# Performance work log

Measured on AMD Instinct MI355X. Metric: run time of the kernel, lower is better.

Reference implementation:

```python
import math
import jax, jax.numpy as jnp
import numpy as np

D_MODEL = 1024
N_HEADS = 16
D_FF = 4096
B = 4
T = 1024  # tgt len
S = 1024  # src len
EPS = 1e-6


def _linear_params(key, d_in, d_out):
    kw, kb = jax.random.split(key)
    w = jax.random.normal(kw, (d_out, d_in), dtype=jnp.float32) * 0.02
    b = jax.random.normal(kb, (d_out,), dtype=jnp.float32) * 0.02
    return w, b


def setup_inputs() -> dict:
    key = jax.random.key(0)
    ks = jax.random.split(key, 16)
    x = jax.random.normal(ks[0], (B, T, D_MODEL), dtype=jnp.float32)
    memory = jax.random.normal(ks[1], (B, S, D_MODEL), dtype=jnp.float32)
    # causal [B, T, T] mask (dim==3 branch) and padding [B, S] mask (dim==2 branch)
    tgt_mask = jnp.broadcast_to(jnp.tril(jnp.ones((T, T), dtype=jnp.int32)), (B, T, T))
    src_mask = jnp.ones((B, S), dtype=jnp.int32)
    inp = {"x": x, "memory": memory, "tgt_mask": tgt_mask, "src_mask": src_mask}
    names = ["sa_wq", "sa_wk", "sa_wv", "sa_wo", "ca_wq", "ca_wk", "ca_wv", "ca_wo"]
    for i, n in enumerate(names):
        w, b = _linear_params(ks[2 + i], D_MODEL, D_MODEL)
        inp[n] = w
        inp[n.replace("w", "b")] = b
    inp["ff_w1"], inp["ff_b1"] = _linear_params(ks[10], D_MODEL, D_FF)
    inp["ff_w2"], inp["ff_b2"] = _linear_params(ks[11], D_FF, D_MODEL)
    for i, n in enumerate(["ln1", "ln2", "ln3"]):
        inp[n + "_w"] = jnp.ones((D_MODEL,), dtype=jnp.float32)
        inp[n + "_b"] = jnp.zeros((D_MODEL,), dtype=jnp.float32)
    return inp


def layernorm(x, w, b):
    # torch-faithful: unbiased std (N-1), eps added to std (not variance)
    mean = jnp.mean(x, axis=-1, keepdims=True)
    d = x - mean
    std = jnp.sqrt(jnp.sum(d * d, axis=-1, keepdims=True) / (x.shape[-1] - 1))
    return w * d / (std + EPS) + b


def mha(q_in, kv_in, mask, wq, bq, wk, bk, wv, bv, wo, bo):
    Bb, Tq, D = q_in.shape
    Tk = kv_in.shape[1]
    dk = D // N_HEADS
    if mask.ndim == 2:
        mask4 = mask[:, None, None, :]
    else:
        mask4 = mask[:, None, :, :]
    q = (q_in @ wq.T + bq).reshape(Bb, Tq, N_HEADS, dk).transpose(0, 2, 1, 3)
    k = (kv_in @ wk.T + bk).reshape(Bb, Tk, N_HEADS, dk).transpose(0, 2, 1, 3)
    v = (kv_in @ wv.T + bv).reshape(Bb, Tk, N_HEADS, dk).transpose(0, 2, 1, 3)
    scores = jnp.einsum("bhqd,bhkd->bhqk", q, k) / math.sqrt(dk)
    scores = jnp.where(mask4 == 0, jnp.float32(-1e9), scores)
    attn = jax.nn.softmax(scores, axis=-1)
    out = jnp.einsum("bhqk,bhkd->bhqd", attn, v)
    out = out.transpose(0, 2, 1, 3).reshape(Bb, Tq, D)
    return out @ wo.T + bo


def reference(x, memory, tgt_mask, src_mask,
              sa_wq, sa_bq, sa_wk, sa_bk, sa_wv, sa_bv, sa_wo, sa_bo,
              ca_wq, ca_bq, ca_wk, ca_bk, ca_wv, ca_bv, ca_wo, ca_bo,
              ff_w1, ff_b1, ff_w2, ff_b2,
              ln1_w, ln1_b, ln2_w, ln2_b, ln3_w, ln3_b):
    # pre-norm decoder block (norm_first=True), dropout=0 (eval)
    h = layernorm(x, ln1_w, ln1_b)
    x = x + mha(h, h, tgt_mask, sa_wq, sa_bq, sa_wk, sa_bk, sa_wv, sa_bv, sa_wo, sa_bo)
    h = layernorm(x, ln2_w, ln2_b)
    x = x + mha(h, memory, src_mask, ca_wq, ca_bq, ca_wk, ca_bk, ca_wv, ca_bv, ca_wo, ca_bo)
    h = layernorm(x, ln3_w, ln3_b)
    x = x + (jax.nn.relu(h @ ff_w1.T + ff_b1) @ ff_w2.T + ff_b2)
    return x
```

## Files before the change

### kernel.cpp

```cpp
#include <hip/hip_runtime.h>
#include <hip/hip_bf16.h>

typedef unsigned short u16;
typedef __attribute__((ext_vector_type(4))) float f32x4;
typedef __attribute__((ext_vector_type(8))) short s16x8;
typedef __attribute__((ext_vector_type(4))) short s16x4;
typedef __attribute__((ext_vector_type(8))) __bf16 bf16x8;

#define NTOK 4096
#define DMODEL 1024
#define DFF 4096
#define NH 16
#define TSEQ 1024

#define SBAR() do { asm volatile("" ::: "memory"); __builtin_amdgcn_s_barrier(); asm volatile("" ::: "memory"); } while (0)


__device__ __forceinline__ u16 f2b_hw(float f) {
  union { __bf16 h; u16 u; } cv;
  cv.h = (__bf16)f;
  return cv.u;
}

__device__ __forceinline__ float b2f(u16 u) {
  return __uint_as_float(((unsigned)u) << 16);
}

__device__ __forceinline__ f32x4 mfma16(s16x8 a, s16x8 b, f32x4 c) {
  return __builtin_amdgcn_mfma_f32_16x16x32_bf16((bf16x8)a, (bf16x8)b, c, 0, 0, 0);
}

__device__ __forceinline__ void gload16(const u16* g, u16* l) {
  __builtin_amdgcn_global_load_lds(
      (const __attribute__((address_space(1))) unsigned int*)g,
      (__attribute__((address_space(3))) unsigned int*)l, 16, 0, 0);
}

__device__ __forceinline__ s16x8 ld8s(const u16* t, int row, int eoff) {
  int rx = row & 7;
  const u16* p1 = t + row * 64 + ((((eoff >> 3) ^ rx) << 3) | (eoff & 7));
  const u16* p2 = t + row * 64 + (((((eoff + 16) >> 3) ^ rx) << 3) | (eoff & 7));
  s16x4 lo = *(const s16x4*)p1;
  s16x4 hi = *(const s16x4*)p2;
  s16x8 r;
  r[0] = lo[0]; r[1] = lo[1]; r[2] = lo[2]; r[3] = lo[3];
  r[4] = hi[0]; r[5] = hi[1]; r[6] = hi[2]; r[7] = hi[3];
  return r;
}

__device__ __forceinline__ s16x8 ld16s(const u16* t, int row, int ch) {
  return *(const s16x8*)(t + row * 64 + ((ch ^ (row & 7)) << 3));
}


struct F2B {
  const float* s[11];
  u16* d[11];
};

__global__ __launch_bounds__(256) void f2b_all(F2B a) {
  int bid = blockIdx.x;
  int seg, boff;
  if (bid < 8192) { seg = bid >> 10; boff = bid & 1023; }
  else { int j = bid - 8192; seg = 8 + (j >> 12); boff = j & 4095; }
  size_t i = ((size_t)boff * 256 + threadIdx.x) * 4;
  float4 v = *(const float4*)(a.s[seg] + i);
  ushort4 o = make_ushort4(f2b_hw(v.x), f2b_hw(v.y), f2b_hw(v.z), f2b_hw(v.w));
  *(ushort4*)(a.d[seg] + i) = o;
}


__global__ __launch_bounds__(256) void ln_kernel(const float* __restrict__ x,
                                                 const float* __restrict__ w,
                                                 const float* __restrict__ b,
                                                 u16* __restrict__ out) {
  int row = blockIdx.x;
  int t = threadIdx.x;
  const float* xr = x + (size_t)row * DMODEL;
  float4 v = *(const float4*)(xr + t * 4);
  float s = v.x + v.y + v.z + v.w;
#pragma unroll
  for (int off = 1; off < 64; off <<= 1) s += __shfl_xor(s, off);
  __shared__ float red[8];
  int wid = t >> 6, lane = t & 63;
  if (lane == 0) red[wid] = s;
  __syncthreads();
  float mean = (red[0] + red[1] + red[2] + red[3]) * (1.0f / 1024.0f);
  float dx = v.x - mean, dy = v.y - mean, dz = v.z - mean, dw = v.w - mean;
  float ss = dx * dx + dy * dy + dz * dz + dw * dw;
#pragma unroll
  for (int off = 1; off < 64; off <<= 1) ss += __shfl_xor(ss, off);
  if (lane == 0) red[4 + wid] = ss;
  __syncthreads();
  float sst = red[4] + red[5] + red[6] + red[7];
  float inv = 1.0f / (sqrtf(sst / 1023.0f) + 1e-6f);
  float4 wv = *(const float4*)(w + t * 4);
  float4 bv = *(const float4*)(b + t * 4);
  ushort4 o = make_ushort4(f2b_hw(wv.x * dx * inv + bv.x), f2b_hw(wv.y * dy * inv + bv.y),
                           f2b_hw(wv.z * dz * inv + bv.z), f2b_hw(wv.w * dw * inv + bv.w));
  *(ushort4*)(out + (size_t)row * DMODEL + t * 4) = o;
}


template <bool RELU>
__global__ __launch_bounds__(512, 2) void gemm256(const u16* __restrict__ A,
                                                  const u16* __restrict__ W,
                                                  const float* __restrict__ bias,
                                                  u16* __restrict__ out,
                                                  int M, int N, int K, int ld,
                                                  int gx) {
  __shared__ u16 As[2][2][8192];
  __shared__ u16 Bs[2][2][8192];
  const int nwg = gridDim.x, qch = nwg >> 3, bid = blockIdx.x;
  const int wg = (bid & 7) * qch + (bid >> 3);
  const int bx = wg % gx, by = wg / gx;
  const int m0 = by * 256, n0 = bx * 256;
  const int tid = threadIdx.x;
  const int wid = tid >> 6, lane = tid & 63;
  const int wr = wid >> 2, wc = wid & 3;
  const int lhi = lane >> 4, llo = lane & 15;
  f32x4 acc[8][4] = {};
  const int srow = tid >> 2;
  const int ssw = ((tid & 3) ^ ((srow >> 1) & 3)) << 3;

  auto unitA = [&](int kt, int kh) {
    const u16* p = A + (size_t)(m0 + srow) * ld + kt * 64 + kh * 32 + ssw;
    gload16(p, &As[kt & 1][kh][tid * 8]);
    gload16(p + (size_t)128 * ld, &As[kt & 1][kh][4096 + tid * 8]);
  };
  auto unitB = [&](int kt, int kh) {
    const u16* p = W + (size_t)(n0 + srow) * ld + kt * 64 + kh * 32 + ssw;
    gload16(p, &Bs[kt & 1][kh][tid * 8]);
    gload16(p + (size_t)128 * ld, &Bs[kt & 1][kh][4096 + tid * 8]);
  };

  s16x8 bf[4];
  auto phase = [&](int d, int ch, int kh, bool loadB, auto stfn, int vm) {
    s16x8 af[4];
#pragma unroll
    for (int fm = 0; fm < 4; fm++) {
      int row = wr * 128 + ch * 64 + fm * 16 + llo;
      af[fm] = *(const s16x8*)(&As[d][kh][row * 32 + ((lhi ^ ((row >> 1) & 3)) << 3)]);
    }
    if (loadB) {
#pragma unroll
      for (int fn = 0; fn < 4; fn++) {
        int row = wc * 64 + fn * 16 + llo;
        bf[fn] = *(const s16x8*)(&Bs[d][kh][row * 32 + ((lhi ^ ((row >> 1) & 3)) << 3)]);
      }
    }
    stfn();
    SBAR();
    __builtin_amdgcn_s_setprio(1);
#pragma unroll
    for (int fm = 0; fm < 4; fm++)
#pragma unroll
      for (int fn = 0; fn < 4; fn++)
        acc[ch * 4 + fm][fn] = mfma16(af[fm], bf[fn], acc[ch * 4 + fm][fn]);
    __builtin_amdgcn_s_setprio(0);
    if (vm == 8) asm volatile("s_waitcnt vmcnt(8)" ::: "memory");
    else if (vm == 4) asm volatile("s_waitcnt vmcnt(4)" ::: "memory");
    else if (vm == 0) asm volatile("s_waitcnt vmcnt(0)" ::: "memory");
    SBAR();
  };

  unitA(0, 0); unitB(0, 0); unitA(0, 1); unitB(0, 1); unitA(1, 0); unitB(1, 0);
  asm volatile("s_waitcnt vmcnt(8)" ::: "memory");
  SBAR();

  const int NPAIR = K >> 7;
#pragma unroll 1
  for (int i = 0; i < NPAIR; ++i) {
    const int tb = 2 * i + 1, tc = 2 * i + 2, td = 2 * i + 3;
    const bool nx = (i + 1 < NPAIR);
    phase(0, 0, 0, true,  [&] { unitA(tb, 1); }, -1);
    phase(0, 1, 0, false, [&] { unitB(tb, 1); }, 8);
    phase(0, 1, 1, true,  [&] { if (nx) unitA(tc, 0); }, -1);
    phase(0, 0, 1, false, [&] { if (nx) unitB(tc, 0); }, nx ? 8 : 4);
    phase(1, 0, 0, true,  [&] { if (nx) unitA(tc, 1); }, -1);
    phase(1, 1, 0, false, [&] { if (nx) unitB(tc, 1); }, nx ? 8 : 0);
    phase(1, 1, 1, true,  [&] { if (nx) unitA(td, 0); }, -1);
    phase(1, 0, 1, false, [&] { if (nx) unitB(td, 0); }, nx ? 8 : -1);
  }

#pragma unroll
  for (int ch = 0; ch < 2; ch++)
#pragma unroll
    for (int fm = 0; fm < 4; fm++)
#pragma unroll
      for (int fn = 0; fn < 4; fn++) {
        int r0 = m0 + wr * 128 + ch * 64 + fm * 16 + lhi * 4;
        int c = n0 + wc * 64 + fn * 16 + llo;
        float bv = bias[c];
#pragma unroll
        for (int i2 = 0; i2 < 4; i2++) {
          float v = acc[ch * 4 + fm][fn][i2] + bv;
          if (RELU) v = fmaxf(v, 0.0f);
          out[(size_t)(r0 + i2) * N + c] = f2b_hw(v);
        }
      }
  (void)M;
}


template <int MODE, bool RELU, bool SPLITK = false, int QBUF = -1, int VBUF = -1>
__global__ __launch_bounds__(512) void gemm_bt(const u16* __restrict__ A,
                                               const u16* __restrict__ A2,
                                               const u16* __restrict__ W,
                                               const float* __restrict__ b0,
                                               const float* __restrict__ b1,
                                               const float* __restrict__ b2,
                                               const float* resid, void* outp,
                                               int M, int N, int K, int ld,
                                               int gx) {
  __shared__ u16 As[2][128 * 64];
  __shared__ u16 Bs[2][128 * 64];
  const int nwg = gridDim.x;
  const int qch = nwg >> 3;
  const int bid = blockIdx.x;
  int wg = (bid & 7) * qch + (bid >> 3);
  int half = 0;
  if (SPLITK) { half = wg & 1; wg >>= 1; }
  const int bx = wg % gx, by = wg / gx;
  const int m0 = by * 128, n0 = bx * 128;
  if (SPLITK) { A += (size_t)half * K; W += (size_t)half * K; }
  if (MODE == 2 && A2 != nullptr && n0 >= 1024) A = A2;
  const int tid = threadIdx.x;
  const int wid = tid >> 6, lane = tid & 63;
  const int wr = wid >> 2, wc = wid & 3;
  const int lhi = lane >> 4, llo = lane & 15;
  f32x4 acc[4][2] = {};
  const int sr = tid >> 3, sc = tid & 7;
  const int srcoff = (sc ^ (sr & 7)) << 3;

  auto stage = [&](int kk, int buf) {
    const u16* Ap = A + (size_t)(m0 + sr) * ld + kk + srcoff;
    gload16(Ap, &As[buf][tid * 8]);
    gload16(Ap + (size_t)64 * ld, &As[buf][4096 + tid * 8]);
    const u16* Wp = W + (size_t)(n0 + sr) * ld + kk + srcoff;
    gload16(Wp, &Bs[buf][tid * 8]);
    gload16(Wp + (size_t)64 * ld, &Bs[buf][4096 + tid * 8]);
  };

  stage(0, 0);
  __syncthreads();

  for (int k0 = 0; k0 < K; k0 += 64) {
    int cur = (k0 >> 6) & 1;
    if (k0 + 64 < K) stage(k0 + 64, cur ^ 1);
#pragma unroll
    for (int ks8 = 0; ks8 < 8; ks8 += 4) {
      s16x8 af[4], bfr[2];
#pragma unroll
      for (int f = 0; f < 4; f++) af[f] = ld16s(&As[cur][0], wr * 64 + f * 16 + llo, ks8 + lhi);
#pragma unroll
      for (int g = 0; g < 2; g++) bfr[g] = ld16s(&Bs[cur][0], wc * 32 + g * 16 + llo, ks8 + lhi);
#pragma unroll
      for (int f = 0; f < 4; f++)
#pragma unroll
        for (int g = 0; g < 2; g++) acc[f][g] = mfma16(af[f], bfr[g], acc[f][g]);
    }
    __syncthreads();
  }

#pragma unroll
  for (int fm = 0; fm < 4; fm++) {
#pragma unroll
    for (int fn = 0; fn < 2; fn++) {
      int c = n0 + wc * 32 + fn * 16 + llo;
      const int r0 = m0 + wr * 64 + fm * 16 + lhi * 4;
      if (MODE == 2) {
        int buf = c >> 10, cc = c & 1023;
        int hh = cc >> 6, d = cc & 63;
        int bb = r0 >> 10, t0 = r0 & 1023;
        const float* bias = (buf == 0) ? b0 : ((buf == 1) ? b1 : b2);
        float bv = bias[cc];
        float v4[4];
#pragma unroll
        for (int i = 0; i < 4; i++) {
          float v = acc[fm][fn][i] + bv;
          if (buf == QBUF) v *= 0.125f;
          v4[i] = v;
        }
        if (buf == VBUF) {
          ushort4 st = make_ushort4(f2b_hw(v4[0]), f2b_hw(v4[1]), f2b_hw(v4[2]), f2b_hw(v4[3]));
          *(ushort4*)(&((u16*)outp)[(size_t)buf * 4194304 +
                                    (((size_t)(bb * NH + hh)) * 64 + d) * TSEQ + t0]) = st;
        } else {
#pragma unroll
          for (int i = 0; i < 4; i++)
            ((u16*)outp)[(size_t)buf * 4194304 +
                         (((size_t)(bb * NH + hh)) * TSEQ + t0 + i) * 64 + d] = f2b_hw(v4[i]);
        }
      } else if (MODE == 4) {
#pragma unroll
        for (int i = 0; i < 4; i++)
          ((u16*)outp)[(size_t)half * M * N + (size_t)(r0 + i) * N + c] =
              f2b_hw(acc[fm][fn][i]);
      } else {
        float bv = b0 ? b0[c] : 0.0f;
#pragma unroll
        for (int i = 0; i < 4; i++) {
          int r = r0 + i;
          float v = acc[fm][fn][i] + bv;
          if (resid) v += resid[(size_t)r * N + c];
          if (RELU) v = fmaxf(v, 0.0f);
          if (MODE == 0) {
            ((float*)outp)[(size_t)r * N + c] = v;
          } else {
            ((u16*)outp)[(size_t)r * N + c] = f2b_hw(v);
          }
        }
      }
    }
  }
}


__global__ __launch_bounds__(256) void ff2_reduce(const u16* __restrict__ p,
                                                  const float* __restrict__ bias,
                                                  float* __restrict__ out) {
  int row = blockIdx.x, t = threadIdx.x;
  size_t i = (size_t)row * 1024 + t * 4;
  const u16* p1 = p + (size_t)4194304;
  s16x4 a = *(const s16x4*)(p + i);
  s16x4 b = *(const s16x4*)(p1 + i);
  float4 r = *(const float4*)(out + i);
  float4 bv = *(const float4*)(bias + t * 4);
  float4 o = make_float4(b2f((u16)a[0]) + b2f((u16)b[0]) + r.x + bv.x,
                         b2f((u16)a[1]) + b2f((u16)b[1]) + r.y + bv.y,
                         b2f((u16)a[2]) + b2f((u16)b[2]) + r.z + bv.z,
                         b2f((u16)a[3]) + b2f((u16)b[3]) + r.w + bv.w);
  *(float4*)(out + i) = o;
}


template <bool CAUSAL>
__global__ __launch_bounds__(256) void attn_kernel(const u16* __restrict__ Qg,
                                                   const u16* __restrict__ Kg,
                                                   const u16* __restrict__ Vt,
                                                   u16* __restrict__ Og) {
  const int bid = blockIdx.x;
  const int wg = (bid & 7) * 64 + (bid >> 3);
  const int bh = wg >> 3;
  const int qblk = (wg & 7) ^ (CAUSAL ? 7 * ((bid >> 8) & 1) : 0);
  const int b = bh >> 4, h = bh & 15;
  const int q0 = qblk * 128;
  const int tid = threadIdx.x, wid = tid >> 6, lane = tid & 63;
  const int lhi = lane >> 4, llo = lane & 15;
  __shared__ u16 Ks[2][4096];
  __shared__ u16 Vs[2][4096];

  const int qr = q0 + wid * 16 + llo;
  const u16* qp0 = Qg + ((size_t)bh * TSEQ + qr) * 64;
  s16x8 qf[2][2];
  qf[0][0] = *(const s16x8*)(qp0 + 8 * lhi);
  qf[0][1] = *(const s16x8*)(qp0 + 8 * (4 + lhi));
  qf[1][0] = *(const s16x8*)(qp0 + 4096 + 8 * lhi);
  qf[1][1] = *(const s16x8*)(qp0 + 4096 + 8 * (4 + lhi));

  f32x4 oacc[2][4] = {};
  float mrun[2] = {-1.0e30f, -1.0e30f}, lrun[2] = {0.0f, 0.0f};
  const size_t kvb = (size_t)bh * (TSEQ * 64);
  const int nt = CAUSAL ? ((q0 + 128) >> 6) : (TSEQ >> 6);

  const int srow = tid >> 3;
  const int ssw = ((tid & 7) ^ (srow & 7)) << 3;

  auto stageK = [&](int s0, int buf) {
    const u16* kb = Kg + kvb + (size_t)s0 * 64;
    gload16(kb + (size_t)srow * 64 + ssw, &Ks[buf][tid * 8]);
    gload16(kb + (size_t)(32 + srow) * 64 + ssw, &Ks[buf][2048 + tid * 8]);
  };
  auto stageV = [&](int s0, int buf) {
    const u16* vb2 = Vt + kvb + s0;
    gload16(vb2 + (size_t)srow * TSEQ + ssw, &Vs[buf][tid * 8]);
    gload16(vb2 + (size_t)(32 + srow) * TSEQ + ssw, &Vs[buf][2048 + tid * 8]);
  };

  stageK(0, 0);
  stageV(0, 0);
  __syncthreads();

  for (int t = 0; t < nt; ++t) {
    int cur = t & 1;
    if (t + 1 < nt) {
      stageK((t + 1) * 64, cur ^ 1);
      stageV((t + 1) * 64, cur ^ 1);
    }
    int s0 = t * 64;
    const bool act0 = !CAUSAL || (s0 < q0 + 64);

    s16x8 kf[4][2];
#pragma unroll
    for (int g = 0; g < 4; g++) {
      kf[g][0] = ld16s(&Ks[cur][0], g * 16 + llo, lhi);
      kf[g][1] = ld16s(&Ks[cur][0], g * 16 + llo, 4 + lhi);
    }

    s16x8 pf[2][2];
#pragma unroll
    for (int s = 0; s < 2; s++) {
      if (s == 0 && !act0) continue;
      f32x4 sacc[4] = {};
#pragma unroll
      for (int g = 0; g < 4; g++) {
        sacc[g] = mfma16(kf[g][0], qf[s][0], sacc[g]);
        sacc[g] = mfma16(kf[g][1], qf[s][1], sacc[g]);
      }
      const int qrow = qr + s * 64;
      const bool diag = CAUSAL && (s0 == q0 + s * 64);
      float sv[16];
      float pmax = -1.0e30f;
#pragma unroll
      for (int g = 0; g < 4; g++)
#pragma unroll
        for (int i = 0; i < 4; i++) {
          float sc = sacc[g][i];
          if (diag) {
            int kv = s0 + g * 16 + lhi * 4 + i;
            if (kv > qrow) sc = -1.0e9f;
          }
          sv[g * 4 + i] = sc;
          pmax = fmaxf(pmax, sc);
        }
      pmax = fmaxf(pmax, __shfl_xor(pmax, 16));
      pmax = fmaxf(pmax, __shfl_xor(pmax, 32));
      if (!__all(pmax - mrun[s] <= 8.0f)) {
        float mnew = fmaxf(mrun[s], pmax);
        float alpha = __expf(mrun[s] - mnew);
        lrun[s] *= alpha;
#pragma unroll
        for (int g = 0; g < 4; g++) {
          oacc[s][g][0] *= alpha; oacc[s][g][1] *= alpha;
          oacc[s][g][2] *= alpha; oacc[s][g][3] *= alpha;
        }
        mrun[s] = mnew;
      }
      float ls = 0.0f;
#pragma unroll
      for (int j = 0; j < 16; j++) {
        float p = __expf(sv[j] - mrun[s]);
        ls += p;
        pf[s][j >> 3][((j >> 2) & 1) * 4 + (j & 3)] = (short)f2b_hw(p);
      }
      ls += __shfl_xor(ls, 16);
      ls += __shfl_xor(ls, 32);
      lrun[s] += ls;
    }

#pragma unroll
    for (int dg = 0; dg < 4; dg++) {
      int row = dg * 16 + llo;
      s16x8 vf0 = ld8s(&Vs[cur][0], row, lhi * 4);
      s16x8 vf1 = ld8s(&Vs[cur][0], row, 32 + lhi * 4);
      if (act0) {
        oacc[0][dg] = mfma16(vf0, pf[0][0], oacc[0][dg]);
        oacc[0][dg] = mfma16(vf1, pf[0][1], oacc[0][dg]);
      }
      oacc[1][dg] = mfma16(vf0, pf[1][0], oacc[1][dg]);
      oacc[1][dg] = mfma16(vf1, pf[1][1], oacc[1][dg]);
    }

    __syncthreads();
  }

#pragma unroll
  for (int s = 0; s < 2; s++) {
    float inv = 1.0f / lrun[s];
    u16* orow = Og + (size_t)(b * TSEQ + qr + s * 64) * DMODEL + h * 64;
#pragma unroll
    for (int dg = 0; dg < 4; dg++) {
      ushort4 st = make_ushort4(f2b_hw(oacc[s][dg][0] * inv), f2b_hw(oacc[s][dg][1] * inv),
                                f2b_hw(oacc[s][dg][2] * inv), f2b_hw(oacc[s][dg][3] * inv));
      *(ushort4*)(orow + dg * 16 + lhi * 4) = st;
    }
  }
}


extern "C" void kernel_launch(void* const* d_in, const int* in_sizes, int n_in,
                              void* d_out, int out_size, void* d_ws, size_t ws_size,
                              hipStream_t stream) {
  const float* x      = (const float*)d_in[0];
  const float* memory = (const float*)d_in[1];
  const float* sa_wq = (const float*)d_in[4];  const float* sa_bq = (const float*)d_in[5];
  const float* sa_wk = (const float*)d_in[6];  const float* sa_bk = (const float*)d_in[7];
  const float* sa_wv = (const float*)d_in[8];  const float* sa_bv = (const float*)d_in[9];
  const float* sa_wo = (const float*)d_in[10]; const float* sa_bo = (const float*)d_in[11];
  const float* ca_wq = (const float*)d_in[12]; const float* ca_bq = (const float*)d_in[13];
  const float* ca_wk = (const float*)d_in[14]; const float* ca_bk = (const float*)d_in[15];
  const float* ca_wv = (const float*)d_in[16]; const float* ca_bv = (const float*)d_in[17];
  const float* ca_wo = (const float*)d_in[18]; const float* ca_bo = (const float*)d_in[19];
  const float* ff_w1 = (const float*)d_in[20]; const float* ff_b1 = (const float*)d_in[21];
  const float* ff_w2 = (const float*)d_in[22]; const float* ff_b2 = (const float*)d_in[23];
  const float* ln1_w = (const float*)d_in[24]; const float* ln1_b = (const float*)d_in[25];
  const float* ln2_w = (const float*)d_in[26]; const float* ln2_b = (const float*)d_in[27];
  const float* ln3_w = (const float*)d_in[28]; const float* ln3_b = (const float*)d_in[29];
  float* out = (float*)d_out;

  char* ws = (char*)d_ws;
  const size_t MB = 1u << 20;
  u16* h_bf   = (u16*)(ws + 0 * MB);
  u16* mem_bf = (u16*)(ws + 8 * MB);
  u16* qb     = (u16*)(ws + 16 * MB);
  u16* kb     = (u16*)(ws + 24 * MB);
  u16* vb     = (u16*)(ws + 32 * MB);
  u16* attnb  = (u16*)(ws + 40 * MB);
  u16* ffmid  = (u16*)(ws + 48 * MB);
  u16* pk     = (u16*)(ws + 16 * MB);
  u16* w_sq   = (u16*)(ws + 80 * MB);
  u16* w_sk   = (u16*)(ws + 82 * MB);
  u16* w_sv   = (u16*)(ws + 84 * MB);
  u16* w_so   = (u16*)(ws + 86 * MB);
  u16* w_cq   = (u16*)(ws + 88 * MB);
  u16* w_ck   = (u16*)(ws + 90 * MB);
  u16* w_cv   = (u16*)(ws + 92 * MB);
  u16* w_co   = (u16*)(ws + 94 * MB);
  u16* w_f1   = (u16*)(ws + 96 * MB);
  u16* w_f2   = (u16*)(ws + 104 * MB);

  F2B fa;
  fa.s[0] = sa_wq; fa.d[0] = w_sq;
  fa.s[1] = sa_wk; fa.d[1] = w_sk;
  fa.s[2] = sa_wv; fa.d[2] = w_sv;
  fa.s[3] = sa_wo; fa.d[3] = w_so;
  fa.s[4] = ca_wq; fa.d[4] = w_cq;
  fa.s[5] = ca_wk; fa.d[5] = w_ck;
  fa.s[6] = ca_wv; fa.d[6] = w_cv;
  fa.s[7] = ca_wo; fa.d[7] = w_co;
  fa.s[8] = ff_w1; fa.d[8] = w_f1;
  fa.s[9] = ff_w2; fa.d[9] = w_f2;
  fa.s[10] = memory; fa.d[10] = mem_bf;
  f2b_all<<<20480, 256, 0, stream>>>(fa);

  ln_kernel<<<4096, 256, 0, stream>>>(x, ln1_w, ln1_b, h_bf);
  gemm_bt<2, false, false, 0, 2><<<768, 512, 0, stream>>>(
      h_bf, nullptr, w_sq, sa_bq, sa_bk, sa_bv, nullptr, qb, NTOK, 3072, DMODEL, DMODEL, 24);
  attn_kernel<true><<<512, 256, 0, stream>>>(qb, kb, vb, attnb);
  gemm_bt<0, false><<<256, 512, 0, stream>>>(attnb, nullptr, w_so, sa_bo, nullptr, nullptr,
                                             x, out, NTOK, DMODEL, DMODEL, DMODEL, 8);

  ln_kernel<<<4096, 256, 0, stream>>>(out, ln2_w, ln2_b, h_bf);
  gemm_bt<2, false, false, 0, 2><<<768, 512, 0, stream>>>(
      h_bf, mem_bf, w_cq, ca_bq, ca_bk, ca_bv, nullptr, qb, NTOK, 3072, DMODEL, DMODEL, 24);
  attn_kernel<false><<<512, 256, 0, stream>>>(qb, kb, vb, attnb);
  gemm_bt<0, false><<<256, 512, 0, stream>>>(attnb, nullptr, w_co, ca_bo, nullptr, nullptr,
                                             out, out, NTOK, DMODEL, DMODEL, DMODEL, 8);

  ln_kernel<<<4096, 256, 0, stream>>>(out, ln3_w, ln3_b, h_bf);
  gemm256<true><<<256, 512, 0, stream>>>(h_bf, w_f1, ff_b1, ffmid,
                                         NTOK, DFF, DMODEL, DMODEL, 16);
  gemm_bt<4, false, true><<<512, 512, 0, stream>>>(ffmid, nullptr, w_f2, nullptr, nullptr,
                                                   nullptr, nullptr, pk, NTOK, DMODEL, 2048, DFF, 8);
  ff2_reduce<<<4096, 256, 0, stream>>>(pk, ff_b2, out);

  (void)in_sizes; (void)n_in; (void)out_size; (void)ws_size;
}
```

Measured before the change: 320.8 us.

## Split attention blocks to 64 query rows, doubling grid size

```diff
diff --git a/kernel.cpp b/kernel.cpp
--- a/kernel.cpp
+++ b/kernel.cpp
@@ -341,11 +341,11 @@
                                                    const u16* __restrict__ Vt,
                                                    u16* __restrict__ Og) {
   const int bid = blockIdx.x;
-  const int wg = (bid & 7) * 64 + (bid >> 3);
-  const int bh = wg >> 3;
-  const int qblk = (wg & 7) ^ (CAUSAL ? 7 * ((bid >> 8) & 1) : 0);
+  const int wg = (bid & 7) * 128 + (bid >> 3);
+  const int bh = wg >> 4;
+  const int qblk = (wg & 15) ^ (CAUSAL ? 15 * ((bid >> 8) & 1) : 0);
   const int b = bh >> 4, h = bh & 15;
-  const int q0 = qblk * 128;
+  const int q0 = qblk * 64;
   const int tid = threadIdx.x, wid = tid >> 6, lane = tid & 63;
   const int lhi = lane >> 4, llo = lane & 15;
   __shared__ u16 Ks[2][4096];
@@ -353,16 +353,13 @@
 
   const int qr = q0 + wid * 16 + llo;
   const u16* qp0 = Qg + ((size_t)bh * TSEQ + qr) * 64;
-  s16x8 qf[2][2];
-  qf[0][0] = *(const s16x8*)(qp0 + 8 * lhi);
-  qf[0][1] = *(const s16x8*)(qp0 + 8 * (4 + lhi));
-  qf[1][0] = *(const s16x8*)(qp0 + 4096 + 8 * lhi);
-  qf[1][1] = *(const s16x8*)(qp0 + 4096 + 8 * (4 + lhi));
-
-  f32x4 oacc[2][4] = {};
-  float mrun[2] = {-1.0e30f, -1.0e30f}, lrun[2] = {0.0f, 0.0f};
+  s16x8 qf0 = *(const s16x8*)(qp0 + 8 * lhi);
+  s16x8 qf1 = *(const s16x8*)(qp0 + 8 * (4 + lhi));
+
+  f32x4 oacc[4] = {};
+  float mrun = -1.0e30f, lrun = 0.0f;
   const size_t kvb = (size_t)bh * (TSEQ * 64);
-  const int nt = CAUSAL ? ((q0 + 128) >> 6) : (TSEQ >> 6);
+  const int nt = CAUSAL ? (qblk + 1) : (TSEQ >> 6);
 
   const int srow = tid >> 3;
   const int ssw = ((tid & 7) ^ (srow & 7)) << 3;
@@ -389,92 +386,72 @@
       stageV((t + 1) * 64, cur ^ 1);
     }
     int s0 = t * 64;
-    const bool act0 = !CAUSAL || (s0 < q0 + 64);
-
-    s16x8 kf[4][2];
+    const bool diag = CAUSAL && (s0 == q0);
+
+    f32x4 sacc[4] = {};
 #pragma unroll
     for (int g = 0; g < 4; g++) {
-      kf[g][0] = ld16s(&Ks[cur][0], g * 16 + llo, lhi);
-      kf[g][1] = ld16s(&Ks[cur][0], g * 16 + llo, 4 + lhi);
-    }
-
-    s16x8 pf[2][2];
-#pragma unroll
-    for (int s = 0; s < 2; s++) {
-      if (s == 0 && !act0) continue;
-      f32x4 sacc[4] = {};
+      int row = g * 16 + llo;
+      sacc[g] = mfma16(ld16s(&Ks[cur][0], row, lhi), qf0, sacc[g]);
+      sacc[g] = mfma16(ld16s(&Ks[cur][0], row, 4 + lhi), qf1, sacc[g]);
+    }
+
+    float sv[16];
+    float pmax = -1.0e30f;
+#pragma unroll
+    for (int g = 0; g < 4; g++)
+#pragma unroll
+      for (int i = 0; i < 4; i++) {
+        float sc = sacc[g][i];
+        if (diag) {
+          int kv = s0 + g * 16 + lhi * 4 + i;
+          if (kv > qr) sc = -1.0e9f;
+        }
+        sv[g * 4 + i] = sc;
+        pmax = fmaxf(pmax, sc);
+      }
+    pmax = fmaxf(pmax, __shfl_xor(pmax, 16));
+    pmax = fmaxf(pmax, __shfl_xor(pmax, 32));
+    if (!__all(pmax - mrun <= 8.0f)) {
+      float mnew = fmaxf(mrun, pmax);
+      float alpha = __expf(mrun - mnew);
+      lrun *= alpha;
 #pragma unroll
       for (int g = 0; g < 4; g++) {
-        sacc[g] = mfma16(kf[g][0], qf[s][0], sacc[g]);
-        sacc[g] = mfma16(kf[g][1], qf[s][1], sacc[g]);
+        oacc[g][0] *= alpha; oacc[g][1] *= alpha;
+        oacc[g][2] *= alpha; oacc[g][3] *= alpha;
       }
-      const int qrow = qr + s * 64;
-      const bool diag = CAUSAL && (s0 == q0 + s * 64);
-      float sv[16];
-      float pmax = -1.0e30f;
-#pragma unroll
-      for (int g = 0; g < 4; g++)
-#pragma unroll
-        for (int i = 0; i < 4; i++) {
-          float sc = sacc[g][i];
-          if (diag) {
-            int kv = s0 + g * 16 + lhi * 4 + i;
-            if (kv > qrow) sc = -1.0e9f;
-          }
-          sv[g * 4 + i] = sc;
-          pmax = fmaxf(pmax, sc);
-        }
-      pmax = fmaxf(pmax, __shfl_xor(pmax, 16));
-      pmax = fmaxf(pmax, __shfl_xor(pmax, 32));
-      if (!__all(pmax - mrun[s] <= 8.0f)) {
-        float mnew = fmaxf(mrun[s], pmax);
-        float alpha = __expf(mrun[s] - mnew);
-        lrun[s] *= alpha;
-#pragma unroll
-        for (int g = 0; g < 4; g++) {
-          oacc[s][g][0] *= alpha; oacc[s][g][1] *= alpha;
-          oacc[s][g][2] *= alpha; oacc[s][g][3] *= alpha;
-        }
-        mrun[s] = mnew;
-      }
-      float ls = 0.0f;
-#pragma unroll
-      for (int j = 0; j < 16; j++) {
-        float p = __expf(sv[j] - mrun[s]);
-        ls += p;
-        pf[s][j >> 3][((j >> 2) & 1) * 4 + (j & 3)] = (short)f2b_hw(p);
-      }
-      ls += __shfl_xor(ls, 16);
-      ls += __shfl_xor(ls, 32);
-      lrun[s] += ls;
-    }
+      mrun = mnew;
+    }
+    s16x8 pf[2];
+    float ls = 0.0f;
+#pragma unroll
+    for (int j = 0; j < 16; j++) {
+      float p = __expf(sv[j] - mrun);
+      ls += p;
+      pf[j >> 3][((j >> 2) & 1) * 4 + (j & 3)] = (short)f2b_hw(p);
+    }
+    ls += __shfl_xor(ls, 16);
+    ls += __shfl_xor(ls, 32);
+    lrun += ls;
 
 #pragma unroll
     for (int dg = 0; dg < 4; dg++) {
       int row = dg * 16 + llo;
-      s16x8 vf0 = ld8s(&Vs[cur][0], row, lhi * 4);
-      s16x8 vf1 = ld8s(&Vs[cur][0], row, 32 + lhi * 4);
-      if (act0) {
-        oacc[0][dg] = mfma16(vf0, pf[0][0], oacc[0][dg]);
-        oacc[0][dg] = mfma16(vf1, pf[0][1], oacc[0][dg]);
-      }
-      oacc[1][dg] = mfma16(vf0, pf[1][0], oacc[1][dg]);
-      oacc[1][dg] = mfma16(vf1, pf[1][1], oacc[1][dg]);
+      oacc[dg] = mfma16(ld8s(&Vs[cur][0], row, lhi * 4), pf[0], oacc[dg]);
+      oacc[dg] = mfma16(ld8s(&Vs[cur][0], row, 32 + lhi * 4), pf[1], oacc[dg]);
     }
 
     __syncthreads();
   }
 
-#pragma unroll
-  for (int s = 0; s < 2; s++) {
-    float inv = 1.0f / lrun[s];
-    u16* orow = Og + (size_t)(b * TSEQ + qr + s * 64) * DMODEL + h * 64;
-#pragma unroll
-    for (int dg = 0; dg < 4; dg++) {
-      ushort4 st = make_ushort4(f2b_hw(oacc[s][dg][0] * inv), f2b_hw(oacc[s][dg][1] * inv),
-                                f2b_hw(oacc[s][dg][2] * inv), f2b_hw(oacc[s][dg][3] * inv));
-      *(ushort4*)(orow + dg * 16 + lhi * 4) = st;
-    }
+  float inv = 1.0f / lrun;
+  u16* orow = Og + (size_t)(b * TSEQ + qr) * DMODEL + h * 64;
+#pragma unroll
+  for (int dg = 0; dg < 4; dg++) {
+    ushort4 st = make_ushort4(f2b_hw(oacc[dg][0] * inv), f2b_hw(oacc[dg][1] * inv),
+                              f2b_hw(oacc[dg][2] * inv), f2b_hw(oacc[dg][3] * inv));
+    *(ushort4*)(orow + dg * 16 + lhi * 4) = st;
   }
 }
 
@@ -537,14 +514,14 @@
   ln_kernel<<<4096, 256, 0, stream>>>(x, ln1_w, ln1_b, h_bf);
   gemm_bt<2, false, false, 0, 2><<<768, 512, 0, stream>>>(
       h_bf, nullptr, w_sq, sa_bq, sa_bk, sa_bv, nullptr, qb, NTOK, 3072, DMODEL, DMODEL, 24);
-  attn_kernel<true><<<512, 256, 0, stream>>>(qb, kb, vb, attnb);
+  attn_kernel<true><<<1024, 256, 0, stream>>>(qb, kb, vb, attnb);
   gemm_bt<0, false><<<256, 512, 0, stream>>>(attnb, nullptr, w_so, sa_bo, nullptr, nullptr,
                                              x, out, NTOK, DMODEL, DMODEL, DMODEL, 8);
 
   ln_kernel<<<4096, 256, 0, stream>>>(out, ln2_w, ln2_b, h_bf);
   gemm_bt<2, false, false, 0, 2><<<768, 512, 0, stream>>>(
       h_bf, mem_bf, w_cq, ca_bq, ca_bk, ca_bv, nullptr, qb, NTOK, 3072, DMODEL, DMODEL, 24);
-  attn_kernel<false><<<512, 256, 0, stream>>>(qb, kb, vb, attnb);
+  attn_kernel<false><<<1024, 256, 0, stream>>>(qb, kb, vb, attnb);
   gemm_bt<0, false><<<256, 512, 0, stream>>>(attnb, nullptr, w_co, ca_bo, nullptr, nullptr,
                                              out, out, NTOK, DMODEL, DMODEL, DMODEL, 8);
 
```

Result: faster. 312.3 us (-2.6%).
